# Kernel optimization log

Hardware: AMD Instinct MI355X
Metric: run time of the kernel (lower is better)

Reference implementation:

```python
import jax, jax.numpy as jnp
import numpy as np

HID = 1024   # hidden_size
NH = 16      # num_heads
HD = HID // NH   # 64 head_dim
RD = int(HD * 0.25)  # 16 rotary_dim
B = 2
S = 2048
ROPE_BASE = 10000.0


def setup_inputs() -> dict:
    key = jax.random.key(0)
    ks = jax.random.split(key, 4)
    hidden_states = jax.random.normal(ks[0], (B, S, HID), jnp.float32)
    # torch nn.Linear weights: [out_features, in_features]
    Wqkv = jax.random.normal(ks[1], (3 * HID, HID), jnp.float32) * (HID ** -0.5)
    bqkv = jnp.zeros((3 * HID,), jnp.float32)
    Wd = jax.random.normal(ks[2], (HID, HID), jnp.float32) * (HID ** -0.5)
    bd = jnp.zeros((HID,), jnp.float32)
    return {"hidden_states": hidden_states, "Wqkv": Wqkv, "bqkv": bqkv, "Wd": Wd, "bd": bd}


def _rotary_tables(seq_len):
    inv_freq = 1.0 / (ROPE_BASE ** (jnp.arange(0, RD, 2, dtype=jnp.float32) / RD))
    t = jnp.arange(seq_len, dtype=jnp.float32)
    freqs = jnp.outer(t, inv_freq)                       # [S, RD/2]
    emb = jnp.concatenate([freqs, freqs], axis=-1)       # [S, RD]
    return jnp.cos(emb)[None, None], jnp.sin(emb)[None, None]  # [1,1,S,RD]


def _rotate_half(x):
    x1, x2 = jnp.split(x, 2, axis=-1)
    return jnp.concatenate([-x2, x1], axis=-1)


def reference(hidden_states, Wqkv, bqkv, Wd, bd):
    b, s, _ = hidden_states.shape
    qkv = hidden_states @ Wqkv.T + bqkv                  # [b,s,3*HID]
    qkv = qkv.reshape(b, s, 3, NH, HD).transpose(2, 0, 3, 1, 4)  # [3,b,nh,s,hd]
    q, k, v = qkv[0], qkv[1], qkv[2]

    cos, sin = _rotary_tables(s)
    q_rot, q_pass = q[..., :RD], q[..., RD:]
    k_rot, k_pass = k[..., :RD], k[..., RD:]
    q_rot = q_rot * cos + _rotate_half(q_rot) * sin
    k_rot = k_rot * cos + _rotate_half(k_rot) * sin
    q = jnp.concatenate([q_rot, q_pass], axis=-1)
    k = jnp.concatenate([k_rot, k_pass], axis=-1)

    scale = HD ** -0.5
    logits = jnp.einsum('bhqd,bhkd->bhqk', q, k) * scale  # [b,nh,s,s]
    causal_mask = jnp.triu(jnp.full((s, s), -jnp.inf, dtype=logits.dtype), 1)
    probs = jax.nn.softmax(logits + causal_mask, axis=-1)

    # KA recurrence: A_i = p_ii * V_i + sum_{j<i} p_ij * A_j
    # <=> (I - strict_lower(P)) A = diag(P) * V  -> batched triangular solve
    L = jnp.eye(s, dtype=probs.dtype) - jnp.tril(probs, -1)      # [b,nh,s,s]
    rhs = jnp.diagonal(probs, axis1=-2, axis2=-1)[..., None] * v  # [b,nh,s,hd]
    A = jax.scipy.linalg.solve_triangular(L, rhs, lower=True)     # [b,nh,s,hd]

    attn_output = A.transpose(0, 2, 1, 3).reshape(b, s, HID)
    return attn_output @ Wd.T + bd
```

## Files before the change

kernel.cpp:

```cpp
#include <hip/hip_runtime.h>
#include <math.h>

namespace {

constexpr int B  = 2, S = 2048, NH = 16, HD = 64, HID = 1024;
constexpr int BH = B * NH;
constexpr int NSTEP = 16;

constexpr size_t OFF_QKV  = 0;
constexpr size_t OFF_PART = 0;
constexpr size_t OFF_A    = 4194304;
constexpr size_t OFF_Q    = 12582912;
constexpr size_t OFF_K    = 16777216;
constexpr size_t OFF_V    = 20971520;
constexpr size_t OFF_ZI   = 25231360;
constexpr size_t OFF_PD   = 25296896;
constexpr size_t OFF_UP   = 25362432;
constexpr size_t WS_FLOATS = 29294592;

typedef __attribute__((ext_vector_type(8))) short bf16x8;
typedef __attribute__((ext_vector_type(4))) float f32x4;

__device__ inline unsigned short bf_rne(float x) {
  const unsigned u = __float_as_uint(x);
  return (unsigned short)((u + 0x7FFFu + ((u >> 16) & 1u)) >> 16);
}
__device__ inline float bf2f(short h) {
  return __uint_as_float((unsigned)(unsigned short)h << 16);
}
__device__ inline float4 ld_hl4(const short* __restrict__ hi,
                                const short* __restrict__ lo, size_t off) {
  const short4 h = *(const short4*)(hi + off);
  const short4 l = *(const short4*)(lo + off);
  return make_float4(bf2f(h.x) + bf2f(l.x), bf2f(h.y) + bf2f(l.y),
                     bf2f(h.z) + bf2f(l.z), bf2f(h.w) + bf2f(l.w));
}
__device__ inline void split8(const float4 a, const float4 b,
                              bf16x8& hi, bf16x8& lo) {
  float v[8] = {a.x, a.y, a.z, a.w, b.x, b.y, b.z, b.w};
#pragma unroll
  for (int i = 0; i < 8; ++i) {
    const unsigned short h = bf_rne(v[i]);
    hi[i] = (short)h;
    lo[i] = (short)bf_rne(v[i] - bf2f((short)h));
  }
}

__global__ __launch_bounds__(256) void split2(
    const float* __restrict__ in, short* __restrict__ hi,
    short* __restrict__ lo, int n4) {
  for (int g = blockIdx.x * 256 + threadIdx.x; g < n4; g += gridDim.x * 256) {
    const float4 x = *(const float4*)(in + (size_t)g * 4);
    short4 h, l;
    h.x = bf_rne(x.x); h.y = bf_rne(x.y); h.z = bf_rne(x.z); h.w = bf_rne(x.w);
    l.x = bf_rne(x.x - bf2f(h.x));
    l.y = bf_rne(x.y - bf2f(h.y));
    l.z = bf_rne(x.z - bf2f(h.z));
    l.w = bf_rne(x.w - bf2f(h.w));
    *(short4*)(hi + (size_t)g * 4) = h;
    *(short4*)(lo + (size_t)g * 4) = l;
  }
}

__global__ __launch_bounds__(256) void split_gather(
    const float* __restrict__ Abuf, short* __restrict__ hi,
    short* __restrict__ lo) {
  const int n4 = B * S * HID / 4;
  for (int g = blockIdx.x * 256 + threadIdx.x; g < n4; g += gridDim.x * 256) {
    const int m = g >> 8, q = g & 255;
    const int k0 = q * 4;
    const int b = m >> 11, s = m & (S - 1);
    const int h = k0 >> 6, d = k0 & 63;
    const float4 x = *(const float4*)(Abuf + (((size_t)(b * NH + h) * S + s) << 6) + d);
    short4 hh, ll;
    hh.x = bf_rne(x.x); hh.y = bf_rne(x.y); hh.z = bf_rne(x.z); hh.w = bf_rne(x.w);
    ll.x = bf_rne(x.x - bf2f(hh.x));
    ll.y = bf_rne(x.y - bf2f(hh.y));
    ll.z = bf_rne(x.z - bf2f(hh.z));
    ll.w = bf_rne(x.w - bf2f(hh.w));
    *(short4*)(hi + (size_t)m * HID + k0) = hh;
    *(short4*)(lo + (size_t)m * HID + k0) = ll;
  }
}

__global__ __launch_bounds__(256) void gemm_bf3(
    const short* __restrict__ Ahi, const short* __restrict__ Alo,
    const short* __restrict__ Bhi, const short* __restrict__ Blo,
    const float* __restrict__ bias, float* __restrict__ C,
    int M, int N, int K) {
  __shared__ short ash[128][40], als[128][40], bsh[128][40], bls[128][40];
  const int t = threadIdx.x;
  const int m0 = blockIdx.y * 128, n0 = blockIdx.x * 128;
  const int w = t >> 6, l = t & 63;
  const int wm = (w >> 1) * 64, wn = (w & 1) * 64;
  const int lr = l & 15, lk = (l >> 4) * 8;
  f32x4 acc[4][4];
#pragma unroll
  for (int i = 0; i < 4; ++i)
#pragma unroll
    for (int j = 0; j < 4; ++j) acc[i][j] = (f32x4)0.f;

  for (int kb = 0; kb < K; kb += 32) {
    __syncthreads();
#pragma unroll
    for (int i = 0; i < 2; ++i) {
      const int idx = t + i * 256;
      const int row = idx >> 2, c8 = (idx & 3) * 8;
      *(uint4*)&ash[row][c8] = *(const uint4*)(Ahi + (size_t)(m0 + row) * K + kb + c8);
      *(uint4*)&als[row][c8] = *(const uint4*)(Alo + (size_t)(m0 + row) * K + kb + c8);
      *(uint4*)&bsh[row][c8] = *(const uint4*)(Bhi + (size_t)(n0 + row) * K + kb + c8);
      *(uint4*)&bls[row][c8] = *(const uint4*)(Blo + (size_t)(n0 + row) * K + kb + c8);
    }
    __syncthreads();
    bf16x8 ah[4], al[4], bh[4], bl[4];
#pragma unroll
    for (int mi = 0; mi < 4; ++mi) {
      ah[mi] = *(const bf16x8*)&ash[wm + mi * 16 + lr][lk];
      al[mi] = *(const bf16x8*)&als[wm + mi * 16 + lr][lk];
    }
#pragma unroll
    for (int ni = 0; ni < 4; ++ni) {
      bh[ni] = *(const bf16x8*)&bsh[wn + ni * 16 + lr][lk];
      bl[ni] = *(const bf16x8*)&bls[wn + ni * 16 + lr][lk];
    }
#pragma unroll
    for (int mi = 0; mi < 4; ++mi)
#pragma unroll
      for (int ni = 0; ni < 4; ++ni) {
        acc[mi][ni] = __builtin_amdgcn_mfma_f32_16x16x32_bf16(
            ah[mi], bh[ni], acc[mi][ni], 0, 0, 0);
        acc[mi][ni] = __builtin_amdgcn_mfma_f32_16x16x32_bf16(
            al[mi], bh[ni], acc[mi][ni], 0, 0, 0);
        acc[mi][ni] = __builtin_amdgcn_mfma_f32_16x16x32_bf16(
            ah[mi], bl[ni], acc[mi][ni], 0, 0, 0);
      }
  }
  const int rq = (l >> 4) * 4;
#pragma unroll
  for (int ni = 0; ni < 4; ++ni) {
    const int col = n0 + wn + ni * 16 + lr;
    const float bv = bias[col];
#pragma unroll
    for (int mi = 0; mi < 4; ++mi)
#pragma unroll
      for (int r = 0; r < 4; ++r) {
        const int row = m0 + wm + mi * 16 + rq + r;
        C[(size_t)row * N + col] = acc[mi][ni][r] + bv;
      }
  }
}

__global__ __launch_bounds__(256) void k2_rope(
    const float* __restrict__ qkv, short* __restrict__ Qhi,
    short* __restrict__ Qlo, short* __restrict__ Khi,
    short* __restrict__ Klo, float* __restrict__ V) {
  const int g  = blockIdx.x * 256 + threadIdx.x;
  const int s  = g & (S - 1);
  const int bh = g >> 11;
  const int b  = bh >> 4, h = bh & 15;
  const float* base = qkv + ((size_t)b * S + s) * 3072 + h * 64;
  float q[64], k[64], v[64];
#pragma unroll
  for (int f = 0; f < 16; ++f) {
    const float4 x = *(const float4*)(base + f * 4);
    q[f*4+0]=x.x; q[f*4+1]=x.y; q[f*4+2]=x.z; q[f*4+3]=x.w;
    const float4 y = *(const float4*)(base + 1024 + f * 4);
    k[f*4+0]=y.x; k[f*4+1]=y.y; k[f*4+2]=y.z; k[f*4+3]=y.w;
    const float4 z = *(const float4*)(base + 2048 + f * 4);
    v[f*4+0]=z.x; v[f*4+1]=z.y; v[f*4+2]=z.z; v[f*4+3]=z.w;
  }
  const float PW[8] = {1.0f, 3.1622776601683795f, 10.0f, 31.622776601683793f,
                       100.0f, 316.22776601683796f, 1000.0f, 3162.2776601683795f};
  float qr[16], kr[16];
#pragma unroll
  for (int d = 0; d < 16; ++d) {
    const int j = d & 7;
    const float invf = 1.0f / PW[j];
    const float fr = (float)s * invf;
    float sn, c;
    sincosf(fr, &sn, &c);
    const float rq = (d < 8) ? -q[d + 8] : q[d - 8];
    const float rk = (d < 8) ? -k[d + 8] : k[d - 8];
    qr[d] = q[d] * c + rq * sn;
    kr[d] = k[d] * c + rk * sn;
  }
#pragma unroll
  for (int d = 0; d < 16; ++d) { q[d] = qr[d]; k[d] = kr[d]; }
#pragma unroll
  for (int d = 0; d < 64; ++d) q[d] *= 0.125f;
  const size_t o = ((size_t)bh * S + s) << 6;
  float* vd = V + o;
#pragma unroll
  for (int f = 0; f < 16; ++f) {
    short4 qh, ql, kh, kl;
    const float* qq = q + f * 4;
    const float* kk = k + f * 4;
    qh.x = bf_rne(qq[0]); qh.y = bf_rne(qq[1]); qh.z = bf_rne(qq[2]); qh.w = bf_rne(qq[3]);
    ql.x = bf_rne(qq[0]-bf2f(qh.x)); ql.y = bf_rne(qq[1]-bf2f(qh.y));
    ql.z = bf_rne(qq[2]-bf2f(qh.z)); ql.w = bf_rne(qq[3]-bf2f(qh.w));
    kh.x = bf_rne(kk[0]); kh.y = bf_rne(kk[1]); kh.z = bf_rne(kk[2]); kh.w = bf_rne(kk[3]);
    kl.x = bf_rne(kk[0]-bf2f(kh.x)); kl.y = bf_rne(kk[1]-bf2f(kh.y));
    kl.z = bf_rne(kk[2]-bf2f(kh.z)); kl.w = bf_rne(kk[3]-bf2f(kh.w));
    *(short4*)(Qhi + o + f*4) = qh;
    *(short4*)(Qlo + o + f*4) = ql;
    *(short4*)(Khi + o + f*4) = kh;
    *(short4*)(Klo + o + f*4) = kl;
    *(float4*)(vd + f*4) = make_float4(v[f*4], v[f*4+1], v[f*4+2], v[f*4+3]);
  }
}

__global__ __launch_bounds__(256) void k3_scores(
    const short* __restrict__ Qhi, const short* __restrict__ Qlo,
    const short* __restrict__ Khi, const short* __restrict__ Klo,
    float* __restrict__ partZ, float* __restrict__ sdg) {
  const int cb = blockIdx.x, rb = blockIdx.y, bh = blockIdx.z;
  if (cb > rb) return;
  __shared__ short qh[128][72], ql[128][72], kh[128][72], kl[128][72];
  __shared__ float red[128][2];
  const int t = threadIdx.x;
  const int w = t >> 6, l = t & 63;
  const int wm = (w >> 1) * 64, wn = (w & 1) * 64;
  const int lr = l & 15, lg = l >> 4;
  for (int v = t; v < 1024; v += 256) {
    const int r = v >> 3, c8 = (v & 7) * 8;
    const size_t gq = (((size_t)bh * S + rb * 128 + r) << 6) + c8;
    const size_t gk = (((size_t)bh * S + cb * 128 + r) << 6) + c8;
    *(uint4*)&qh[r][c8] = *(const uint4*)(Qhi + gq);
    *(uint4*)&ql[r][c8] = *(const uint4*)(Qlo + gq);
    *(uint4*)&kh[r][c8] = *(const uint4*)(Khi + gk);
    *(uint4*)&kl[r][c8] = *(const uint4*)(Klo + gk);
  }
  __syncthreads();
  f32x4 acc[4][4];
#pragma unroll
  for (int i = 0; i < 4; ++i)
#pragma unroll
    for (int j = 0; j < 4; ++j) acc[i][j] = (f32x4)0.f;
#pragma unroll
  for (int ks = 0; ks < 2; ++ks) {
    const int lk = ks * 32 + lg * 8;
    bf16x8 ah[4], al[4], bhf[4], blf[4];
#pragma unroll
    for (int mi = 0; mi < 4; ++mi) {
      ah[mi] = *(const bf16x8*)&qh[wm + mi * 16 + lr][lk];
      al[mi] = *(const bf16x8*)&ql[wm + mi * 16 + lr][lk];
    }
#pragma unroll
    for (int ni = 0; ni < 4; ++ni) {
      bhf[ni] = *(const bf16x8*)&kh[wn + ni * 16 + lr][lk];
      blf[ni] = *(const bf16x8*)&kl[wn + ni * 16 + lr][lk];
    }
#pragma unroll
    for (int mi = 0; mi < 4; ++mi)
#pragma unroll
      for (int ni = 0; ni < 4; ++ni) {
        acc[mi][ni] = __builtin_amdgcn_mfma_f32_16x16x32_bf16(
            ah[mi], bhf[ni], acc[mi][ni], 0, 0, 0);
        acc[mi][ni] = __builtin_amdgcn_mfma_f32_16x16x32_bf16(
            al[mi], bhf[ni], acc[mi][ni], 0, 0, 0);
        acc[mi][ni] = __builtin_amdgcn_mfma_f32_16x16x32_bf16(
            ah[mi], blf[ni], acc[mi][ni], 0, 0, 0);
      }
  }
  const int rq = lg * 4;
  const int rowbase = rb * 128 + wm, colbase = cb * 128 + wn;
  float rp[4][4];
#pragma unroll
  for (int mi = 0; mi < 4; ++mi)
#pragma unroll
    for (int r = 0; r < 4; ++r) rp[mi][r] = 0.f;
#pragma unroll
  for (int mi = 0; mi < 4; ++mi)
#pragma unroll
    for (int ni = 0; ni < 4; ++ni)
#pragma unroll
      for (int r = 0; r < 4; ++r) {
        const int rG = rowbase + mi * 16 + rq + r;
        const int cG = colbase + ni * 16 + lr;
        if (cG <= rG) rp[mi][r] += __expf(acc[mi][ni][r]);
        if (cG == rG) sdg[(size_t)bh * S + rG] = acc[mi][ni][r];
      }
#pragma unroll
  for (int off = 1; off < 16; off <<= 1)
#pragma unroll
    for (int mi = 0; mi < 4; ++mi)
#pragma unroll
      for (int r = 0; r < 4; ++r)
        rp[mi][r] += __shfl_xor(rp[mi][r], off, 64);
  if (lr == 0)
#pragma unroll
    for (int mi = 0; mi < 4; ++mi)
#pragma unroll
      for (int r = 0; r < 4; ++r)
        red[wm + mi * 16 + rq + r][w & 1] = rp[mi][r];
  __syncthreads();
  if (t < 128)
    partZ[(((size_t)bh * 16 + rb) * 16 + cb) * 128 + t] = red[t][0] + red[t][1];
}

__global__ __launch_bounds__(256) void k3_reduce(
    const float* __restrict__ partZ, float* __restrict__ zinv,
    float* __restrict__ pdg) {
  const int R = blockIdx.x * 256 + threadIdx.x;
  const int bh = R >> 11, r = R & 2047;
  const int rb = r >> 7, row = r & 127;
  float Z = 0.f;
  for (int c = 0; c <= rb; ++c)
    Z += partZ[(((size_t)bh*16 + rb)*16 + c)*128 + row];
  const float zi = 1.f / Z;
  zinv[R] = zi;
  pdg[R] = __expf(pdg[R]) * zi;
}

__global__ __launch_bounds__(256) void k4_minv(
    const short* __restrict__ Qhi, const short* __restrict__ Qlo,
    const short* __restrict__ Khi, const short* __restrict__ Klo,
    const float* __restrict__ zinv, short* __restrict__ Mrh,
    short* __restrict__ Mrl, short* __restrict__ P10h,
    short* __restrict__ P10l) {
  const int bh = blockIdx.y, ib = blockIdx.x;
  const int r0 = ib * 64;
  __shared__ float Nb[64][68];
  __shared__ float X[64][68];
  const int t = threadIdx.x;
  const int w = t >> 6, l = t & 63;
  const int lr = l & 15, lg = l >> 4;

  bf16x8 qfh[2], qfl[2];
  const size_t qbase = (((size_t)bh * S + r0 + 16 * w + lr) << 6);
#pragma unroll
  for (int ks = 0; ks < 2; ++ks) {
    qfh[ks] = *(const bf16x8*)(Qhi + qbase + ks * 32 + lg * 8);
    qfl[ks] = *(const bf16x8*)(Qlo + qbase + ks * 32 + lg * 8);
  }
  const int rloc0 = 16 * w + lg * 4;
  float ziv[4];
#pragma unroll
  for (int i = 0; i < 4; ++i) ziv[i] = zinv[(size_t)bh * S + r0 + rloc0 + i];

  {
    f32x4 acc[4];
#pragma unroll
    for (int i = 0; i < 4; ++i) acc[i] = (f32x4)0.f;
    const size_t kbase = ((size_t)bh * S + r0) << 6;
#pragma unroll
    for (int ks = 0; ks < 2; ++ks) {
#pragma unroll
      for (int ni = 0; ni < 4; ++ni) {
        const size_t kb = kbase + (((size_t)(16 * ni + lr)) << 6) + ks * 32 + lg * 8;
        const bf16x8 bhf = *(const bf16x8*)(Khi + kb);
        const bf16x8 blf = *(const bf16x8*)(Klo + kb);
        acc[ni] = __builtin_amdgcn_mfma_f32_16x16x32_bf16(qfh[ks], bhf, acc[ni], 0, 0, 0);
        acc[ni] = __builtin_amdgcn_mfma_f32_16x16x32_bf16(qfl[ks], bhf, acc[ni], 0, 0, 0);
        acc[ni] = __builtin_amdgcn_mfma_f32_16x16x32_bf16(qfh[ks], blf, acc[ni], 0, 0, 0);
      }
    }
#pragma unroll
    for (int ni = 0; ni < 4; ++ni) {
      const int c = 16 * ni + lr;
#pragma unroll
      for (int i = 0; i < 4; ++i) {
        const int r = rloc0 + i;
        Nb[r][c] = (c < r) ? __expf(acc[ni][i]) * ziv[i] : 0.f;
      }
    }
  }
  if (ib & 1) {
    f32x4 p[4];
#pragma unroll
    for (int i = 0; i < 4; ++i) p[i] = (f32x4)0.f;
    const size_t kbase = ((size_t)bh * S + r0 - 64) << 6;
#pragma unroll
    for (int ks = 0; ks < 2; ++ks) {
#pragma unroll
      for (int ni = 0; ni < 4; ++ni) {
        const size_t kb = kbase + (((size_t)(16 * ni + lr)) << 6) + ks * 32 + lg * 8;
        const bf16x8 bhf = *(const bf16x8*)(Khi + kb);
        const bf16x8 blf = *(const bf16x8*)(Klo + kb);
        p[ni] = __builtin_amdgcn_mfma_f32_16x16x32_bf16(qfh[ks], bhf, p[ni], 0, 0, 0);
        p[ni] = __builtin_amdgcn_mfma_f32_16x16x32_bf16(qfl[ks], bhf, p[ni], 0, 0, 0);
        p[ni] = __builtin_amdgcn_mfma_f32_16x16x32_bf16(qfh[ks], blf, p[ni], 0, 0, 0);
      }
    }
    const size_t pbase = (((size_t)bh * 16 + (ib >> 1)) * 64) * 64;
#pragma unroll
    for (int ni = 0; ni < 4; ++ni) {
      const int c = 16 * ni + lr;
#pragma unroll
      for (int i = 0; i < 4; ++i) {
        const float val = __expf(p[ni][i]) * ziv[i];
        const unsigned short h = bf_rne(val);
        P10h[pbase + (size_t)(rloc0 + i) * 64 + c] = (short)h;
        P10l[pbase + (size_t)(rloc0 + i) * 64 + c] = (short)bf_rne(val - bf2f((short)h));
      }
    }
  }
  {
    const int c = t & 63, g = t >> 6;
#pragma unroll
    for (int i = 0; i < 16; ++i) {
      const int r = 16 * g + i;
      X[r][c] = (r == c) ? 1.f : 0.f;
    }
  }
  __syncthreads();

  const int c = t & 63, g = t >> 6;
  if (w == 0) {
    for (int rr = 1; rr < 16; ++rr) {
      float a = 0.f;
      for (int j = 0; j < rr; ++j) a += Nb[rr][j] * X[j][l];
      X[rr][l] += a;
    }
  }
  __syncthreads();
#pragma unroll
  for (int I = 1; I < 4; ++I) {
    {
      const int rb4 = 16 * I + 4 * g;
      float s0 = 0.f, s1 = 0.f, s2 = 0.f, s3 = 0.f;
      for (int j = 0; j < 16 * I; j += 4) {
        const float4 n0 = *(const float4*)&Nb[rb4 + 0][j];
        const float4 n1 = *(const float4*)&Nb[rb4 + 1][j];
        const float4 n2 = *(const float4*)&Nb[rb4 + 2][j];
        const float4 n3 = *(const float4*)&Nb[rb4 + 3][j];
        const float x0 = X[j + 0][c], x1 = X[j + 1][c];
        const float x2 = X[j + 2][c], x3 = X[j + 3][c];
        s0 += n0.x * x0 + n0.y * x1 + n0.z * x2 + n0.w * x3;
        s1 += n1.x * x0 + n1.y * x1 + n1.z * x2 + n1.w * x3;
        s2 += n2.x * x0 + n2.y * x1 + n2.z * x2 + n2.w * x3;
        s3 += n3.x * x0 + n3.y * x1 + n3.z * x2 + n3.w * x3;
      }
      X[rb4 + 0][c] += s0; X[rb4 + 1][c] += s1;
      X[rb4 + 2][c] += s2; X[rb4 + 3][c] += s3;
    }
    __syncthreads();
    if (w == 0) {
      const int rb = 16 * I;
      for (int rr = 1; rr < 16; ++rr) {
        const int r = rb + rr;
        float a = 0.f;
        for (int j = rb; j < r; ++j) a += Nb[r][j] * X[j][l];
        X[r][l] += a;
      }
    }
    __syncthreads();
  }

  const size_t mb = (((size_t)bh * 32 + ib) * 64) * 64;
  for (int v = t; v < 4096; v += 256) {
    const int r = v >> 6, cc = v & 63;
    const float x = X[r][cc];
    const unsigned short h = bf_rne(x);
    Mrh[mb + v] = (short)h;
    Mrl[mb + v] = (short)bf_rne(x - bf2f((short)h));
  }
}

__global__ __launch_bounds__(256) void k5_acc(
    const short* __restrict__ Qhi, const short* __restrict__ Qlo,
    const short* __restrict__ Khi, const short* __restrict__ Klo,
    const float* __restrict__ Abuf, const float* __restrict__ zinv,
    float* __restrict__ upart, int kstep) {
  const int bh = blockIdx.y, j = blockIdx.x;
  __shared__ float Es[128][68];
  __shared__ float Ats[64][68];
  const int t = threadIdx.x;
  const int w = t >> 6, l = t & 63;
  const int lr = l & 15, lg = l >> 4;
  const int rw = 32 * w;
  const int base = kstep * 128;

  bf16x8 qfh[2][2], qfl[2][2];
#pragma unroll
  for (int mi = 0; mi < 2; ++mi)
#pragma unroll
    for (int ks = 0; ks < 2; ++ks) {
      const size_t qo = (((size_t)bh * S + base + rw + mi * 16 + lr) << 6) + ks * 32 + lg * 8;
      qfh[mi][ks] = *(const bf16x8*)(Qhi + qo);
      qfl[mi][ks] = *(const bf16x8*)(Qlo + qo);
    }
  float ziv[2][4];
#pragma unroll
  for (int mi = 0; mi < 2; ++mi)
#pragma unroll
    for (int r = 0; r < 4; ++r)
      ziv[mi][r] = zinv[(size_t)bh * S + base + rw + mi * 16 + lg * 4 + r];

  f32x4 out[2][4];
#pragma unroll
  for (int mi = 0; mi < 2; ++mi)
#pragma unroll
    for (int ni = 0; ni < 4; ++ni) out[mi][ni] = (f32x4)0.f;

  for (int h = 0; h < 2; ++h) {
    __syncthreads();
    for (int v = t; v < 1024; v += 256) {
      const int d = v & 63, sq = v >> 6;
      const size_t ab = ((size_t)bh * S + j * 128 + h * 64 + sq * 4) << 6;
      float4 o;
      o.x = Abuf[ab + d];
      o.y = Abuf[ab + 64 + d];
      o.z = Abuf[ab + 128 + d];
      o.w = Abuf[ab + 192 + d];
      *(float4*)&Ats[d][sq * 4] = o;
    }
    f32x4 qk[2][4];
#pragma unroll
    for (int mi = 0; mi < 2; ++mi)
#pragma unroll
      for (int ni = 0; ni < 4; ++ni) qk[mi][ni] = (f32x4)0.f;
#pragma unroll
    for (int ks = 0; ks < 2; ++ks) {
#pragma unroll
      for (int ni = 0; ni < 4; ++ni) {
        const size_t ko = (((size_t)bh * S + j * 128 + h * 64 + ni * 16 + lr) << 6) + ks * 32 + lg * 8;
        const bf16x8 kh8 = *(const bf16x8*)(Khi + ko);
        const bf16x8 kl8 = *(const bf16x8*)(Klo + ko);
#pragma unroll
        for (int mi = 0; mi < 2; ++mi) {
          qk[mi][ni] = __builtin_amdgcn_mfma_f32_16x16x32_bf16(
              qfh[mi][ks], kh8, qk[mi][ni], 0, 0, 0);
          qk[mi][ni] = __builtin_amdgcn_mfma_f32_16x16x32_bf16(
              qfl[mi][ks], kh8, qk[mi][ni], 0, 0, 0);
          qk[mi][ni] = __builtin_amdgcn_mfma_f32_16x16x32_bf16(
              qfh[mi][ks], kl8, qk[mi][ni], 0, 0, 0);
        }
      }
    }
#pragma unroll
    for (int mi = 0; mi < 2; ++mi)
#pragma unroll
      for (int ni = 0; ni < 4; ++ni)
#pragma unroll
        for (int r = 0; r < 4; ++r)
          Es[rw + mi * 16 + lg * 4 + r][ni * 16 + lr] =
              __expf(qk[mi][ni][r]) * ziv[mi][r];
    __syncthreads();
#pragma unroll
    for (int ks = 0; ks < 2; ++ks) {
      bf16x8 eh[2], el[2];
#pragma unroll
      for (int mi = 0; mi < 2; ++mi) {
        const float* ep = &Es[rw + mi * 16 + lr][ks * 32 + lg * 8];
        split8(*(const float4*)ep, *(const float4*)(ep + 4), eh[mi], el[mi]);
      }
#pragma unroll
      for (int ni = 0; ni < 4; ++ni) {
        const float* ap = &Ats[ni * 16 + lr][ks * 32 + lg * 8];
        bf16x8 ah8, al8;
        split8(*(const float4*)ap, *(const float4*)(ap + 4), ah8, al8);
#pragma unroll
        for (int mi = 0; mi < 2; ++mi) {
          out[mi][ni] = __builtin_amdgcn_mfma_f32_16x16x32_bf16(
              eh[mi], ah8, out[mi][ni], 0, 0, 0);
          out[mi][ni] = __builtin_amdgcn_mfma_f32_16x16x32_bf16(
              el[mi], ah8, out[mi][ni], 0, 0, 0);
          out[mi][ni] = __builtin_amdgcn_mfma_f32_16x16x32_bf16(
              eh[mi], al8, out[mi][ni], 0, 0, 0);
        }
      }
    }
  }
  float* ub = upart + (((size_t)bh * 15 + j) * 128) * 64;
#pragma unroll
  for (int mi = 0; mi < 2; ++mi)
#pragma unroll
    for (int ni = 0; ni < 4; ++ni)
#pragma unroll
      for (int r = 0; r < 4; ++r)
        ub[(size_t)(rw + mi * 16 + lg * 4 + r) * 64 + ni * 16 + lr] =
            out[mi][ni][r];
}

__global__ __launch_bounds__(256) void k5_fin(
    const float* __restrict__ V, const float* __restrict__ pd,
    const float* __restrict__ upart, const short* __restrict__ Mrh,
    const short* __restrict__ Mrl, const short* __restrict__ P10h,
    const short* __restrict__ P10l, float* __restrict__ Abuf, int kstep) {
  const int d0 = blockIdx.x * 16;
  const int bh = blockIdx.y;
  const int t = threadIdx.x;
  const int w = t >> 6, l = t & 63;
  const int lr = l & 15, lg = l >> 4;
  const int base = kstep * 128;
  __shared__ float uT[16][132];
  __shared__ float aT[16][68];

  for (int v = t; v < 512; v += 256) {
    const int r = v >> 2, f = v & 3;
    const int R = base + r;
    const float4 x = *(const float4*)(V + (((size_t)bh * S + R) << 6) + d0 + f * 4);
    const float p = pd[(size_t)bh * S + R];
    float a0 = p * x.x, a1 = p * x.y, a2 = p * x.z, a3 = p * x.w;
    for (int j = 0; j < kstep; ++j) {
      const float4 y = *(const float4*)(
          upart + ((((size_t)bh * 15 + j) * 128 + r) << 6) + d0 + f * 4);
      a0 += y.x; a1 += y.y; a2 += y.z; a3 += y.w;
    }
    uT[f * 4 + 0][r] = a0; uT[f * 4 + 1][r] = a1;
    uT[f * 4 + 2][r] = a2; uT[f * 4 + 3][r] = a3;
  }
  __syncthreads();
  {
    f32x4 o = (f32x4)0.f;
    const size_t mb = (((size_t)bh * 32 + kstep * 2) * 64 + 16 * w + lr) * 64;
#pragma unroll
    for (int ks = 0; ks < 2; ++ks) {
      const bf16x8 mh = *(const bf16x8*)(Mrh + mb + ks * 32 + lg * 8);
      const bf16x8 ml = *(const bf16x8*)(Mrl + mb + ks * 32 + lg * 8);
      const float* up_ = &uT[lr][ks * 32 + lg * 8];
      bf16x8 uh, ul;
      split8(*(const float4*)up_, *(const float4*)(up_ + 4), uh, ul);
      o = __builtin_amdgcn_mfma_f32_16x16x32_bf16(mh, uh, o, 0, 0, 0);
      o = __builtin_amdgcn_mfma_f32_16x16x32_bf16(ml, uh, o, 0, 0, 0);
      o = __builtin_amdgcn_mfma_f32_16x16x32_bf16(mh, ul, o, 0, 0, 0);
    }
#pragma unroll
    for (int i = 0; i < 4; ++i) {
      const int r = 16 * w + lg * 4 + i;
      Abuf[(((size_t)bh * S + base + r) << 6) + d0 + lr] = o[i];
      aT[lr][r] = o[i];
    }
  }
  __syncthreads();
  {
    f32x4 o = (f32x4)0.f;
    const size_t pb = (((size_t)bh * 16 + kstep) * 64 + 16 * w + lr) * 64;
#pragma unroll
    for (int ks = 0; ks < 2; ++ks) {
      const bf16x8 ph = *(const bf16x8*)(P10h + pb + ks * 32 + lg * 8);
      const bf16x8 pl = *(const bf16x8*)(P10l + pb + ks * 32 + lg * 8);
      const float* ap = &aT[lr][ks * 32 + lg * 8];
      bf16x8 ah, al;
      split8(*(const float4*)ap, *(const float4*)(ap + 4), ah, al);
      o = __builtin_amdgcn_mfma_f32_16x16x32_bf16(ph, ah, o, 0, 0, 0);
      o = __builtin_amdgcn_mfma_f32_16x16x32_bf16(pl, ah, o, 0, 0, 0);
      o = __builtin_amdgcn_mfma_f32_16x16x32_bf16(ph, al, o, 0, 0, 0);
    }
#pragma unroll
    for (int i = 0; i < 4; ++i)
      uT[lr][64 + 16 * w + lg * 4 + i] += o[i];
  }
  __syncthreads();
  {
    f32x4 o = (f32x4)0.f;
    const size_t mb = (((size_t)bh * 32 + kstep * 2 + 1) * 64 + 16 * w + lr) * 64;
#pragma unroll
    for (int ks = 0; ks < 2; ++ks) {
      const bf16x8 mh = *(const bf16x8*)(Mrh + mb + ks * 32 + lg * 8);
      const bf16x8 ml = *(const bf16x8*)(Mrl + mb + ks * 32 + lg * 8);
      const float* up_ = &uT[lr][64 + ks * 32 + lg * 8];
      bf16x8 uh, ul;
      split8(*(const float4*)up_, *(const float4*)(up_ + 4), uh, ul);
      o = __builtin_amdgcn_mfma_f32_16x16x32_bf16(mh, uh, o, 0, 0, 0);
      o = __builtin_amdgcn_mfma_f32_16x16x32_bf16(ml, uh, o, 0, 0, 0);
      o = __builtin_amdgcn_mfma_f32_16x16x32_bf16(mh, ul, o, 0, 0, 0);
    }
#pragma unroll
    for (int i = 0; i < 4; ++i) {
      const int r = 16 * w + lg * 4 + i;
      Abuf[(((size_t)bh * S + base + 64 + r) << 6) + d0 + lr] = o[i];
    }
  }
}

}

extern "C" void kernel_launch(void* const* d_in, const int* in_sizes, int n_in,
                              void* d_out, int out_size, void* d_ws, size_t ws_size,
                              hipStream_t stream) {
  const float* hs   = (const float*)d_in[0];
  const float* Wqkv = (const float*)d_in[1];
  const float* bqkv = (const float*)d_in[2];
  const float* Wd   = (const float*)d_in[3];
  const float* bd   = (const float*)d_in[4];
  float* out = (float*)d_out;
  float* W   = (float*)d_ws;
  if (ws_size < WS_FLOATS * sizeof(float)) return;

  float* qkv   = W + OFF_QKV;
  float* partZ = W + OFF_PART;
  float* Abuf  = W + OFF_A;
  short* Qhi   = (short*)(W + OFF_Q);
  short* Qlo   = Qhi + 4194304;
  short* Khi   = (short*)(W + OFF_K);
  short* Klo   = Khi + 4194304;
  float* Vb    = W + OFF_V;
  float* zi    = W + OFF_ZI;
  float* pdg   = W + OFF_PD;
  float* up    = W + OFF_UP;

  char* wsb = (char*)d_ws;
  short* Ahi  = (short*)(wsb + 50331648);
  short* Alo  = Ahi + 4194304;
  short* Whi  = (short*)(wsb + 67108864);
  short* Wlo  = Whi + 3145728;
  short* A2hi = (short*)(wsb + 50331648);
  short* A2lo = A2hi + 4194304;
  short* Wdhi = (short*)(wsb + 67108864);
  short* Wdlo = Wdhi + 1048576;
  short* P10h = (short*)(wsb);
  short* P10l = P10h + 2097152;
  short* Mrh  = (short*)(wsb + 33554432);
  short* Mrl  = Mrh + 4194304;

  split2<<<dim3(2048), 256, 0, stream>>>(hs, Ahi, Alo, B*S*HID/4);
  split2<<<dim3(2048), 256, 0, stream>>>(Wqkv, Whi, Wlo, 3*HID*HID/4);
  gemm_bf3<<<dim3(24, 32), 256, 0, stream>>>(Ahi, Alo, Whi, Wlo, bqkv, qkv,
                                             B*S, 3*HID, HID);
  k2_rope<<<dim3(BH * S / 256), 256, 0, stream>>>(qkv, Qhi, Qlo, Khi, Klo, Vb);
  k3_scores<<<dim3(16, 16, BH), 256, 0, stream>>>(Qhi, Qlo, Khi, Klo, partZ, pdg);
  k3_reduce<<<dim3(BH * S / 256), 256, 0, stream>>>(partZ, zi, pdg);
  k4_minv<<<dim3(S / 64, BH), 256, 0, stream>>>(Qhi, Qlo, Khi, Klo, zi,
                                                Mrh, Mrl, P10h, P10l);
  for (int k = 0; k < NSTEP; ++k) {
    if (k > 0)
      k5_acc<<<dim3(k, BH), 256, 0, stream>>>(Qhi, Qlo, Khi, Klo, Abuf, zi, up, k);
    k5_fin<<<dim3(4, BH), 256, 0, stream>>>(Vb, pdg, up, Mrh, Mrl, P10h, P10l,
                                            Abuf, k);
  }
  split_gather<<<dim3(2048), 256, 0, stream>>>(Abuf, A2hi, A2lo);
  split2<<<dim3(2048), 256, 0, stream>>>(Wd, Wdhi, Wdlo, HID*HID/4);
  gemm_bf3<<<dim3(8, 32), 256, 0, stream>>>(A2hi, A2lo, Wdhi, Wdlo, bd, out,
                                            B*S, HID, HID);
}
```

Measured before the change: 738.9 us.

## Process 256-row steps in blocked triangular solve, halving sequential launches

The blocked forward substitution now advances 256 rows per step instead of 128, so the serial k5_acc/k5_fin launch chain drops from 16 to 8 iterations. k5_fin solves the two 128-row halves itself, computing the in-step off-diagonal block with MFMA. k5_acc caps its grid at 7 blocks per row half and loops over column tiles, which bounds how many partial sums k5_fin has to reduce. The split kernels are also merged pairwise to cut launches. The cost is that k5_fin now does much more serial work while only 128 blocks are active.

Result: faster. 692.5 us (-6.3%).

```diff
diff --git a/kernel.cpp b/kernel.cpp
--- a/kernel.cpp
+++ b/kernel.cpp
@@ -5,10 +5,8 @@
 
 constexpr int B  = 2, S = 2048, NH = 16, HD = 64, HID = 1024;
 constexpr int BH = B * NH;
-constexpr int NSTEP = 16;
-
-constexpr size_t OFF_QKV  = 0;
-constexpr size_t OFF_PART = 0;
+constexpr int NSTEP2 = 8;
+
 constexpr size_t OFF_A    = 4194304;
 constexpr size_t OFF_Q    = 12582912;
 constexpr size_t OFF_K    = 16777216;
@@ -28,13 +26,6 @@
 __device__ inline float bf2f(short h) {
   return __uint_as_float((unsigned)(unsigned short)h << 16);
 }
-__device__ inline float4 ld_hl4(const short* __restrict__ hi,
-                                const short* __restrict__ lo, size_t off) {
-  const short4 h = *(const short4*)(hi + off);
-  const short4 l = *(const short4*)(lo + off);
-  return make_float4(bf2f(h.x) + bf2f(l.x), bf2f(h.y) + bf2f(l.y),
-                     bf2f(h.z) + bf2f(l.z), bf2f(h.w) + bf2f(l.w));
-}
 __device__ inline void split8(const float4 a, const float4 b,
                               bf16x8& hi, bf16x8& lo) {
   float v[8] = {a.x, a.y, a.z, a.w, b.x, b.y, b.z, b.w};
@@ -45,41 +36,79 @@
     lo[i] = (short)bf_rne(v[i] - bf2f((short)h));
   }
 }
-
-__global__ __launch_bounds__(256) void split2(
-    const float* __restrict__ in, short* __restrict__ hi,
-    short* __restrict__ lo, int n4) {
-  for (int g = blockIdx.x * 256 + threadIdx.x; g < n4; g += gridDim.x * 256) {
-    const float4 x = *(const float4*)(in + (size_t)g * 4);
+__device__ inline f32x4 apply3(const short* __restrict__ mh_,
+                               const short* __restrict__ ml_,
+                               const float* __restrict__ brow, int lg) {
+  f32x4 o = (f32x4)0.f;
+#pragma unroll
+  for (int ks = 0; ks < 2; ++ks) {
+    const bf16x8 mh = *(const bf16x8*)(mh_ + ks * 32 + lg * 8);
+    const bf16x8 ml = *(const bf16x8*)(ml_ + ks * 32 + lg * 8);
+    const float* bp = brow + ks * 32 + lg * 8;
+    bf16x8 bh, bl;
+    split8(*(const float4*)bp, *(const float4*)(bp + 4), bh, bl);
+    o = __builtin_amdgcn_mfma_f32_16x16x32_bf16(mh, bh, o, 0, 0, 0);
+    o = __builtin_amdgcn_mfma_f32_16x16x32_bf16(ml, bh, o, 0, 0, 0);
+    o = __builtin_amdgcn_mfma_f32_16x16x32_bf16(mh, bl, o, 0, 0, 0);
+  }
+  return o;
+}
+
+__global__ __launch_bounds__(256) void split_pre(
+    const float* __restrict__ hs, short* __restrict__ h1, short* __restrict__ l1,
+    const float* __restrict__ wq, short* __restrict__ h2, short* __restrict__ l2) {
+  const int n1 = B * S * HID / 4;
+  const int n2 = 3 * HID * HID / 4;
+  for (int g = blockIdx.x * 256 + threadIdx.x; g < n1 + n2; g += gridDim.x * 256) {
+    const bool first = g < n1;
+    const int idx = first ? g : g - n1;
+    const float4 x = first ? *(const float4*)(hs + (size_t)idx * 4)
+                           : *(const float4*)(wq + (size_t)idx * 4);
     short4 h, l;
     h.x = bf_rne(x.x); h.y = bf_rne(x.y); h.z = bf_rne(x.z); h.w = bf_rne(x.w);
     l.x = bf_rne(x.x - bf2f(h.x));
     l.y = bf_rne(x.y - bf2f(h.y));
     l.z = bf_rne(x.z - bf2f(h.z));
     l.w = bf_rne(x.w - bf2f(h.w));
-    *(short4*)(hi + (size_t)g * 4) = h;
-    *(short4*)(lo + (size_t)g * 4) = l;
-  }
-}
-
-__global__ __launch_bounds__(256) void split_gather(
-    const float* __restrict__ Abuf, short* __restrict__ hi,
-    short* __restrict__ lo) {
-  const int n4 = B * S * HID / 4;
-  for (int g = blockIdx.x * 256 + threadIdx.x; g < n4; g += gridDim.x * 256) {
-    const int m = g >> 8, q = g & 255;
-    const int k0 = q * 4;
-    const int b = m >> 11, s = m & (S - 1);
-    const int h = k0 >> 6, d = k0 & 63;
-    const float4 x = *(const float4*)(Abuf + (((size_t)(b * NH + h) * S + s) << 6) + d);
-    short4 hh, ll;
-    hh.x = bf_rne(x.x); hh.y = bf_rne(x.y); hh.z = bf_rne(x.z); hh.w = bf_rne(x.w);
-    ll.x = bf_rne(x.x - bf2f(hh.x));
-    ll.y = bf_rne(x.y - bf2f(hh.y));
-    ll.z = bf_rne(x.z - bf2f(hh.z));
-    ll.w = bf_rne(x.w - bf2f(hh.w));
-    *(short4*)(hi + (size_t)m * HID + k0) = hh;
-    *(short4*)(lo + (size_t)m * HID + k0) = ll;
+    if (first) {
+      *(short4*)(h1 + (size_t)idx * 4) = h;
+      *(short4*)(l1 + (size_t)idx * 4) = l;
+    } else {
+      *(short4*)(h2 + (size_t)idx * 4) = h;
+      *(short4*)(l2 + (size_t)idx * 4) = l;
+    }
+  }
+}
+
+__global__ __launch_bounds__(256) void split_post(
+    const float* __restrict__ Abuf, short* __restrict__ h1, short* __restrict__ l1,
+    const float* __restrict__ wd, short* __restrict__ h2, short* __restrict__ l2) {
+  const int n1 = B * S * HID / 4;
+  const int n2 = HID * HID / 4;
+  for (int g = blockIdx.x * 256 + threadIdx.x; g < n1 + n2; g += gridDim.x * 256) {
+    float4 x;
+    if (g < n1) {
+      const int m = g >> 8, q = g & 255;
+      const int k0 = q * 4;
+      const int b = m >> 11, s = m & (S - 1);
+      const int h = k0 >> 6, d = k0 & 63;
+      x = *(const float4*)(Abuf + (((size_t)(b * NH + h) * S + s) << 6) + d);
+    } else {
+      x = *(const float4*)(wd + (size_t)(g - n1) * 4);
+    }
+    short4 h, l;
+    h.x = bf_rne(x.x); h.y = bf_rne(x.y); h.z = bf_rne(x.z); h.w = bf_rne(x.w);
+    l.x = bf_rne(x.x - bf2f(h.x));
+    l.y = bf_rne(x.y - bf2f(h.y));
+    l.z = bf_rne(x.z - bf2f(h.z));
+    l.w = bf_rne(x.w - bf2f(h.w));
+    if (g < n1) {
+      *(short4*)(h1 + (size_t)g * 4) = h;
+      *(short4*)(l1 + (size_t)g * 4) = l;
+    } else {
+      *(short4*)(h2 + (size_t)(g - n1) * 4) = h;
+      *(short4*)(l2 + (size_t)(g - n1) * 4) = l;
+    }
   }
 }
 
@@ -461,15 +490,15 @@
     const short* __restrict__ Qhi, const short* __restrict__ Qlo,
     const short* __restrict__ Khi, const short* __restrict__ Klo,
     const float* __restrict__ Abuf, const float* __restrict__ zinv,
-    float* __restrict__ upart, int kstep) {
-  const int bh = blockIdx.y, j = blockIdx.x;
+    float* __restrict__ up, int s) {
+  const int bh = blockIdx.z, rh = blockIdx.y, g = blockIdx.x;
   __shared__ float Es[128][68];
   __shared__ float Ats[64][68];
   const int t = threadIdx.x;
   const int w = t >> 6, l = t & 63;
   const int lr = l & 15, lg = l >> 4;
   const int rw = 32 * w;
-  const int base = kstep * 128;
+  const int base = s * 256 + rh * 128;
 
   bf16x8 qfh[2][2], qfl[2][2];
 #pragma unroll
@@ -493,76 +522,78 @@
 #pragma unroll
     for (int ni = 0; ni < 4; ++ni) out[mi][ni] = (f32x4)0.f;
 
-  for (int h = 0; h < 2; ++h) {
-    __syncthreads();
-    for (int v = t; v < 1024; v += 256) {
-      const int d = v & 63, sq = v >> 6;
-      const size_t ab = ((size_t)bh * S + j * 128 + h * 64 + sq * 4) << 6;
-      float4 o;
-      o.x = Abuf[ab + d];
-      o.y = Abuf[ab + 64 + d];
-      o.z = Abuf[ab + 128 + d];
-      o.w = Abuf[ab + 192 + d];
-      *(float4*)&Ats[d][sq * 4] = o;
-    }
-    f32x4 qk[2][4];
-#pragma unroll
-    for (int mi = 0; mi < 2; ++mi)
-#pragma unroll
-      for (int ni = 0; ni < 4; ++ni) qk[mi][ni] = (f32x4)0.f;
-#pragma unroll
-    for (int ks = 0; ks < 2; ++ks) {
-#pragma unroll
-      for (int ni = 0; ni < 4; ++ni) {
-        const size_t ko = (((size_t)bh * S + j * 128 + h * 64 + ni * 16 + lr) << 6) + ks * 32 + lg * 8;
-        const bf16x8 kh8 = *(const bf16x8*)(Khi + ko);
-        const bf16x8 kl8 = *(const bf16x8*)(Klo + ko);
+  for (int j = g; j < 2 * s; j += 7) {
+    for (int h = 0; h < 2; ++h) {
+      __syncthreads();
+      for (int v = t; v < 1024; v += 256) {
+        const int d = v & 63, sq = v >> 6;
+        const size_t ab = ((size_t)bh * S + j * 128 + h * 64 + sq * 4) << 6;
+        float4 o;
+        o.x = Abuf[ab + d];
+        o.y = Abuf[ab + 64 + d];
+        o.z = Abuf[ab + 128 + d];
+        o.w = Abuf[ab + 192 + d];
+        *(float4*)&Ats[d][sq * 4] = o;
+      }
+      f32x4 qk[2][4];
+#pragma unroll
+      for (int mi = 0; mi < 2; ++mi)
+#pragma unroll
+        for (int ni = 0; ni < 4; ++ni) qk[mi][ni] = (f32x4)0.f;
+#pragma unroll
+      for (int ks = 0; ks < 2; ++ks) {
+#pragma unroll
+        for (int ni = 0; ni < 4; ++ni) {
+          const size_t ko = (((size_t)bh * S + j * 128 + h * 64 + ni * 16 + lr) << 6) + ks * 32 + lg * 8;
+          const bf16x8 kh8 = *(const bf16x8*)(Khi + ko);
+          const bf16x8 kl8 = *(const bf16x8*)(Klo + ko);
+#pragma unroll
+          for (int mi = 0; mi < 2; ++mi) {
+            qk[mi][ni] = __builtin_amdgcn_mfma_f32_16x16x32_bf16(
+                qfh[mi][ks], kh8, qk[mi][ni], 0, 0, 0);
+            qk[mi][ni] = __builtin_amdgcn_mfma_f32_16x16x32_bf16(
+                qfl[mi][ks], kh8, qk[mi][ni], 0, 0, 0);
+            qk[mi][ni] = __builtin_amdgcn_mfma_f32_16x16x32_bf16(
+                qfh[mi][ks], kl8, qk[mi][ni], 0, 0, 0);
+          }
+        }
+      }
+#pragma unroll
+      for (int mi = 0; mi < 2; ++mi)
+#pragma unroll
+        for (int ni = 0; ni < 4; ++ni)
+#pragma unroll
+          for (int r = 0; r < 4; ++r)
+            Es[rw + mi * 16 + lg * 4 + r][ni * 16 + lr] =
+                __expf(qk[mi][ni][r]) * ziv[mi][r];
+      __syncthreads();
+#pragma unroll
+      for (int ks = 0; ks < 2; ++ks) {
+        bf16x8 eh[2], el[2];
 #pragma unroll
         for (int mi = 0; mi < 2; ++mi) {
-          qk[mi][ni] = __builtin_amdgcn_mfma_f32_16x16x32_bf16(
-              qfh[mi][ks], kh8, qk[mi][ni], 0, 0, 0);
-          qk[mi][ni] = __builtin_amdgcn_mfma_f32_16x16x32_bf16(
-              qfl[mi][ks], kh8, qk[mi][ni], 0, 0, 0);
-          qk[mi][ni] = __builtin_amdgcn_mfma_f32_16x16x32_bf16(
-              qfh[mi][ks], kl8, qk[mi][ni], 0, 0, 0);
+          const float* ep = &Es[rw + mi * 16 + lr][ks * 32 + lg * 8];
+          split8(*(const float4*)ep, *(const float4*)(ep + 4), eh[mi], el[mi]);
         }
-      }
-    }
-#pragma unroll
-    for (int mi = 0; mi < 2; ++mi)
-#pragma unroll
-      for (int ni = 0; ni < 4; ++ni)
-#pragma unroll
-        for (int r = 0; r < 4; ++r)
-          Es[rw + mi * 16 + lg * 4 + r][ni * 16 + lr] =
-              __expf(qk[mi][ni][r]) * ziv[mi][r];
-    __syncthreads();
-#pragma unroll
-    for (int ks = 0; ks < 2; ++ks) {
-      bf16x8 eh[2], el[2];
-#pragma unroll
-      for (int mi = 0; mi < 2; ++mi) {
-        const float* ep = &Es[rw + mi * 16 + lr][ks * 32 + lg * 8];
-        split8(*(const float4*)ep, *(const float4*)(ep + 4), eh[mi], el[mi]);
-      }
-#pragma unroll
-      for (int ni = 0; ni < 4; ++ni) {
-        const float* ap = &Ats[ni * 16 + lr][ks * 32 + lg * 8];
-        bf16x8 ah8, al8;
-        split8(*(const float4*)ap, *(const float4*)(ap + 4), ah8, al8);
-#pragma unroll
-        for (int mi = 0; mi < 2; ++mi) {
-          out[mi][ni] = __builtin_amdgcn_mfma_f32_16x16x32_bf16(
-              eh[mi], ah8, out[mi][ni], 0, 0, 0);
-          out[mi][ni] = __builtin_amdgcn_mfma_f32_16x16x32_bf16(
-              el[mi], ah8, out[mi][ni], 0, 0, 0);
-          out[mi][ni] = __builtin_amdgcn_mfma_f32_16x16x32_bf16(
-              eh[mi], al8, out[mi][ni], 0, 0, 0);
+#pragma unroll
+        for (int ni = 0; ni < 4; ++ni) {
+          const float* ap = &Ats[ni * 16 + lr][ks * 32 + lg * 8];
+          bf16x8 ah8, al8;
+          split8(*(const float4*)ap, *(const float4*)(ap + 4), ah8, al8);
+#pragma unroll
+          for (int mi = 0; mi < 2; ++mi) {
+            out[mi][ni] = __builtin_amdgcn_mfma_f32_16x16x32_bf16(
+                eh[mi], ah8, out[mi][ni], 0, 0, 0);
+            out[mi][ni] = __builtin_amdgcn_mfma_f32_16x16x32_bf16(
+                el[mi], ah8, out[mi][ni], 0, 0, 0);
+            out[mi][ni] = __builtin_amdgcn_mfma_f32_16x16x32_bf16(
+                eh[mi], al8, out[mi][ni], 0, 0, 0);
+          }
         }
       }
     }
   }
-  float* ub = upart + (((size_t)bh * 15 + j) * 128) * 64;
+  float* ub = up + (((size_t)(bh * 7 + g) * 2 + rh) << 13);
 #pragma unroll
   for (int mi = 0; mi < 2; ++mi)
 #pragma unroll
@@ -574,48 +605,44 @@
 }
 
 __global__ __launch_bounds__(256) void k5_fin(
+    const short* __restrict__ Qhi, const short* __restrict__ Qlo,
+    const short* __restrict__ Khi, const short* __restrict__ Klo,
     const float* __restrict__ V, const float* __restrict__ pd,
-    const float* __restrict__ upart, const short* __restrict__ Mrh,
-    const short* __restrict__ Mrl, const short* __restrict__ P10h,
-    const short* __restrict__ P10l, float* __restrict__ Abuf, int kstep) {
+    const float* __restrict__ zinv, const float* __restrict__ up,
+    const short* __restrict__ Mrh, const short* __restrict__ Mrl,
+    const short* __restrict__ P10h, const short* __restrict__ P10l,
+    float* __restrict__ Abuf, int s) {
   const int d0 = blockIdx.x * 16;
   const int bh = blockIdx.y;
   const int t = threadIdx.x;
   const int w = t >> 6, l = t & 63;
   const int lr = l & 15, lg = l >> 4;
-  const int base = kstep * 128;
-  __shared__ float uT[16][132];
-  __shared__ float aT[16][68];
-
-  for (int v = t; v < 512; v += 256) {
+  const int base = s * 256;
+  __shared__ float uT[16][260];
+  __shared__ float aT[16][132];
+  __shared__ float Es[128][68];
+  const int ng = (2 * s < 7) ? 2 * s : 7;
+
+  for (int v = t; v < 1024; v += 256) {
     const int r = v >> 2, f = v & 3;
     const int R = base + r;
     const float4 x = *(const float4*)(V + (((size_t)bh * S + R) << 6) + d0 + f * 4);
     const float p = pd[(size_t)bh * S + R];
     float a0 = p * x.x, a1 = p * x.y, a2 = p * x.z, a3 = p * x.w;
-    for (int j = 0; j < kstep; ++j) {
+    const int rh = r >> 7, rr = r & 127;
+    for (int g = 0; g < ng; ++g) {
       const float4 y = *(const float4*)(
-          upart + ((((size_t)bh * 15 + j) * 128 + r) << 6) + d0 + f * 4);
+          up + (((size_t)(bh * 7 + g) * 2 + rh) << 13) + (rr << 6) + d0 + f * 4);
       a0 += y.x; a1 += y.y; a2 += y.z; a3 += y.w;
     }
     uT[f * 4 + 0][r] = a0; uT[f * 4 + 1][r] = a1;
     uT[f * 4 + 2][r] = a2; uT[f * 4 + 3][r] = a3;
   }
   __syncthreads();
+  const size_t mstep = (size_t)bh * 32 + s * 4;
   {
-    f32x4 o = (f32x4)0.f;
-    const size_t mb = (((size_t)bh * 32 + kstep * 2) * 64 + 16 * w + lr) * 64;
-#pragma unroll
-    for (int ks = 0; ks < 2; ++ks) {
-      const bf16x8 mh = *(const bf16x8*)(Mrh + mb + ks * 32 + lg * 8);
-      const bf16x8 ml = *(const bf16x8*)(Mrl + mb + ks * 32 + lg * 8);
-      const float* up_ = &uT[lr][ks * 32 + lg * 8];
-      bf16x8 uh, ul;
-      split8(*(const float4*)up_, *(const float4*)(up_ + 4), uh, ul);
-      o = __builtin_amdgcn_mfma_f32_16x16x32_bf16(mh, uh, o, 0, 0, 0);
-      o = __builtin_amdgcn_mfma_f32_16x16x32_bf16(ml, uh, o, 0, 0, 0);
-      o = __builtin_amdgcn_mfma_f32_16x16x32_bf16(mh, ul, o, 0, 0, 0);
-    }
+    const size_t mb = ((mstep + 0) * 64 + 16 * w + lr) * 64;
+    const f32x4 o = apply3(Mrh + mb, Mrl + mb, &uT[lr][0], lg);
 #pragma unroll
     for (int i = 0; i < 4; ++i) {
       const int r = 16 * w + lg * 4 + i;
@@ -625,42 +652,122 @@
   }
   __syncthreads();
   {
-    f32x4 o = (f32x4)0.f;
-    const size_t pb = (((size_t)bh * 16 + kstep) * 64 + 16 * w + lr) * 64;
-#pragma unroll
-    for (int ks = 0; ks < 2; ++ks) {
-      const bf16x8 ph = *(const bf16x8*)(P10h + pb + ks * 32 + lg * 8);
-      const bf16x8 pl = *(const bf16x8*)(P10l + pb + ks * 32 + lg * 8);
-      const float* ap = &aT[lr][ks * 32 + lg * 8];
-      bf16x8 ah, al;
-      split8(*(const float4*)ap, *(const float4*)(ap + 4), ah, al);
-      o = __builtin_amdgcn_mfma_f32_16x16x32_bf16(ph, ah, o, 0, 0, 0);
-      o = __builtin_amdgcn_mfma_f32_16x16x32_bf16(pl, ah, o, 0, 0, 0);
-      o = __builtin_amdgcn_mfma_f32_16x16x32_bf16(ph, al, o, 0, 0, 0);
-    }
+    const size_t pb = (((size_t)bh * 16 + 2 * s) * 64 + 16 * w + lr) * 64;
+    const f32x4 o = apply3(P10h + pb, P10l + pb, &aT[lr][0], lg);
 #pragma unroll
     for (int i = 0; i < 4; ++i)
       uT[lr][64 + 16 * w + lg * 4 + i] += o[i];
   }
   __syncthreads();
   {
-    f32x4 o = (f32x4)0.f;
-    const size_t mb = (((size_t)bh * 32 + kstep * 2 + 1) * 64 + 16 * w + lr) * 64;
-#pragma unroll
-    for (int ks = 0; ks < 2; ++ks) {
-      const bf16x8 mh = *(const bf16x8*)(Mrh + mb + ks * 32 + lg * 8);
-      const bf16x8 ml = *(const bf16x8*)(Mrl + mb + ks * 32 + lg * 8);
-      const float* up_ = &uT[lr][64 + ks * 32 + lg * 8];
-      bf16x8 uh, ul;
-      split8(*(const float4*)up_, *(const float4*)(up_ + 4), uh, ul);
-      o = __builtin_amdgcn_mfma_f32_16x16x32_bf16(mh, uh, o, 0, 0, 0);
-      o = __builtin_amdgcn_mfma_f32_16x16x32_bf16(ml, uh, o, 0, 0, 0);
-      o = __builtin_amdgcn_mfma_f32_16x16x32_bf16(mh, ul, o, 0, 0, 0);
-    }
+    const size_t mb = ((mstep + 1) * 64 + 16 * w + lr) * 64;
+    const f32x4 o = apply3(Mrh + mb, Mrl + mb, &uT[lr][64], lg);
 #pragma unroll
     for (int i = 0; i < 4; ++i) {
       const int r = 16 * w + lg * 4 + i;
       Abuf[(((size_t)bh * S + base + 64 + r) << 6) + d0 + lr] = o[i];
+      aT[lr][64 + r] = o[i];
+    }
+  }
+  {
+    const int rw = 32 * w;
+    bf16x8 qh_[2][2], ql_[2][2];
+#pragma unroll
+    for (int mi = 0; mi < 2; ++mi)
+#pragma unroll
+      for (int ks = 0; ks < 2; ++ks) {
+        const size_t qo = (((size_t)bh * S + base + 128 + rw + mi * 16 + lr) << 6) + ks * 32 + lg * 8;
+        qh_[mi][ks] = *(const bf16x8*)(Qhi + qo);
+        ql_[mi][ks] = *(const bf16x8*)(Qlo + qo);
+      }
+    float zv[2][4];
+#pragma unroll
+    for (int mi = 0; mi < 2; ++mi)
+#pragma unroll
+      for (int i = 0; i < 4; ++i)
+        zv[mi][i] = zinv[(size_t)bh * S + base + 128 + rw + mi * 16 + lg * 4 + i];
+    for (int ch = 0; ch < 2; ++ch) {
+      __syncthreads();
+      f32x4 qk[2][4];
+#pragma unroll
+      for (int mi = 0; mi < 2; ++mi)
+#pragma unroll
+        for (int ni = 0; ni < 4; ++ni) qk[mi][ni] = (f32x4)0.f;
+#pragma unroll
+      for (int ks = 0; ks < 2; ++ks) {
+#pragma unroll
+        for (int ni = 0; ni < 4; ++ni) {
+          const size_t ko = (((size_t)bh * S + base + ch * 64 + ni * 16 + lr) << 6) + ks * 32 + lg * 8;
+          const bf16x8 kh8 = *(const bf16x8*)(Khi + ko);
+          const bf16x8 kl8 = *(const bf16x8*)(Klo + ko);
+#pragma unroll
+          for (int mi = 0; mi < 2; ++mi) {
+            qk[mi][ni] = __builtin_amdgcn_mfma_f32_16x16x32_bf16(
+                qh_[mi][ks], kh8, qk[mi][ni], 0, 0, 0);
+            qk[mi][ni] = __builtin_amdgcn_mfma_f32_16x16x32_bf16(
+                ql_[mi][ks], kh8, qk[mi][ni], 0, 0, 0);
+            qk[mi][ni] = __builtin_amdgcn_mfma_f32_16x16x32_bf16(
+                qh_[mi][ks], kl8, qk[mi][ni], 0, 0, 0);
+          }
+        }
+      }
+#pragma unroll
+      for (int mi = 0; mi < 2; ++mi)
+#pragma unroll
+        for (int ni = 0; ni < 4; ++ni)
+#pragma unroll
+          for (int i = 0; i < 4; ++i)
+            Es[rw + mi * 16 + lg * 4 + i][ni * 16 + lr] =
+                __expf(qk[mi][ni][i]) * zv[mi][i];
+      __syncthreads();
+#pragma unroll
+      for (int mi = 0; mi < 2; ++mi) {
+        f32x4 o = (f32x4)0.f;
+#pragma unroll
+        for (int kq = 0; kq < 2; ++kq) {
+          const float* ep = &Es[rw + mi * 16 + lr][kq * 32 + lg * 8];
+          bf16x8 eh, el;
+          split8(*(const float4*)ep, *(const float4*)(ep + 4), eh, el);
+          const float* ap = &aT[lr][ch * 64 + kq * 32 + lg * 8];
+          bf16x8 ah, al;
+          split8(*(const float4*)ap, *(const float4*)(ap + 4), ah, al);
+          o = __builtin_amdgcn_mfma_f32_16x16x32_bf16(eh, ah, o, 0, 0, 0);
+          o = __builtin_amdgcn_mfma_f32_16x16x32_bf16(el, ah, o, 0, 0, 0);
+          o = __builtin_amdgcn_mfma_f32_16x16x32_bf16(eh, al, o, 0, 0, 0);
+        }
+#pragma unroll
+        for (int i = 0; i < 4; ++i)
+          uT[lr][128 + rw + mi * 16 + lg * 4 + i] += o[i];
+      }
+    }
+  }
+  __syncthreads();
+  {
+    const size_t mb = ((mstep + 2) * 64 + 16 * w + lr) * 64;
+    const f32x4 o = apply3(Mrh + mb, Mrl + mb, &uT[lr][128], lg);
+#pragma unroll
+    for (int i = 0; i < 4; ++i) {
+      const int r = 16 * w + lg * 4 + i;
+      Abuf[(((size_t)bh * S + base + 128 + r) << 6) + d0 + lr] = o[i];
+      aT[lr][r] = o[i];
+    }
+  }
+  __syncthreads();
+  {
+    const size_t pb = (((size_t)bh * 16 + 2 * s + 1) * 64 + 16 * w + lr) * 64;
+    const f32x4 o = apply3(P10h + pb, P10l + pb, &aT[lr][0], lg);
+#pragma unroll
+    for (int i = 0; i < 4; ++i)
+      uT[lr][192 + 16 * w + lg * 4 + i] += o[i];
+  }
+  __syncthreads();
+  {
+    const size_t mb = ((mstep + 3) * 64 + 16 * w + lr) * 64;
+    const f32x4 o = apply3(Mrh + mb, Mrl + mb, &uT[lr][192], lg);
+#pragma unroll
+    for (int i = 0; i < 4; ++i) {
+      const int r = 16 * w + lg * 4 + i;
+      Abuf[(((size_t)bh * S + base + 192 + r) << 6) + d0 + lr] = o[i];
     }
   }
 }
@@ -679,8 +786,8 @@
   float* W   = (float*)d_ws;
   if (ws_size < WS_FLOATS * sizeof(float)) return;
 
-  float* qkv   = W + OFF_QKV;
-  float* partZ = W + OFF_PART;
+  float* qkv   = W;
+  float* partZ = W;
   float* Abuf  = W + OFF_A;
   short* Qhi   = (short*)(W + OFF_Q);
   short* Qlo   = Qhi + 4194304;
@@ -705,8 +812,7 @@
   short* Mrh  = (short*)(wsb + 33554432);
   short* Mrl  = Mrh + 4194304;
 
-  split2<<<dim3(2048), 256, 0, stream>>>(hs, Ahi, Alo, B*S*HID/4);
-  split2<<<dim3(2048), 256, 0, stream>>>(Wqkv, Whi, Wlo, 3*HID*HID/4);
+  split_pre<<<dim3(2048), 256, 0, stream>>>(hs, Ahi, Alo, Wqkv, Whi, Wlo);
   gemm_bf3<<<dim3(24, 32), 256, 0, stream>>>(Ahi, Alo, Whi, Wlo, bqkv, qkv,
                                              B*S, 3*HID, HID);
   k2_rope<<<dim3(BH * S / 256), 256, 0, stream>>>(qkv, Qhi, Qlo, Khi, Klo, Vb);
@@ -714,14 +820,16 @@
   k3_reduce<<<dim3(BH * S / 256), 256, 0, stream>>>(partZ, zi, pdg);
   k4_minv<<<dim3(S / 64, BH), 256, 0, stream>>>(Qhi, Qlo, Khi, Klo, zi,
                                                 Mrh, Mrl, P10h, P10l);
-  for (int k = 0; k < NSTEP; ++k) {
-    if (k > 0)
-      k5_acc<<<dim3(k, BH), 256, 0, stream>>>(Qhi, Qlo, Khi, Klo, Abuf, zi, up, k);
-    k5_fin<<<dim3(4, BH), 256, 0, stream>>>(Vb, pdg, up, Mrh, Mrl, P10h, P10l,
-                                            Abuf, k);
-  }
-  split_gather<<<dim3(2048), 256, 0, stream>>>(Abuf, A2hi, A2lo);
-  split2<<<dim3(2048), 256, 0, stream>>>(Wd, Wdhi, Wdlo, HID*HID/4);
+  for (int s = 0; s < NSTEP2; ++s) {
+    if (s > 0) {
+      const int ng = (2 * s < 7) ? 2 * s : 7;
+      k5_acc<<<dim3(ng, 2, BH), 256, 0, stream>>>(Qhi, Qlo, Khi, Klo, Abuf, zi,
+                                                  up, s);
+    }
+    k5_fin<<<dim3(4, BH), 256, 0, stream>>>(Qhi, Qlo, Khi, Klo, Vb, pdg, zi, up,
+                                            Mrh, Mrl, P10h, P10l, Abuf, s);
+  }
+  split_post<<<dim3(2048), 256, 0, stream>>>(Abuf, A2hi, A2lo, Wd, Wdhi, Wdlo);
   gemm_bf3<<<dim3(8, 32), 256, 0, stream>>>(A2hi, A2lo, Wdhi, Wdlo, bd, out,
                                             B*S, HID, HID);
 }
```
